# Performance work log

Hardware: AMD Instinct MI355X
Metric: run time of the kernel (lower is better)

Reference implementation:

```python
import jax, jax.numpy as jnp
import numpy as np

BLK = 128            # weight_block_size for w8a16 blockwise dequant
H = 1024             # hidden_size
I = 512              # moe_intermediate_size
E = 64               # n_routed_experts
T = 512              # tokens (seq_len)
K = 6                # num_experts_per_tok
G = 8                # n_group
TG = 3               # topk_group
NSH = 2              # n_shared_experts
I2 = I * NSH         # shared expert intermediate size
ROUTED_SCALE = 2.5
NORM_TOPK = True


def dq(w_int8, scale, blk=BLK):
    """Blockwise w8a16 dequant: w [..., M, N] int8, scale [..., M/blk, N/blk] f32."""
    *lead, M, N = w_int8.shape
    w = w_int8.astype(scale.dtype).reshape(*lead, M // blk, blk, N // blk, blk)
    return (w * scale[..., :, None, :, None]).reshape(*lead, M, N)


def setup_inputs() -> dict:
    key = jax.random.key(0)
    ks = jax.random.split(key, 16)
    ri = lambda k, shp: jax.random.randint(k, shp, -8, 8, dtype=jnp.int8)
    rs = lambda k, shp: jax.random.uniform(k, shp, minval=0.01, maxval=0.03, dtype=jnp.float32)
    return {
        "x": jax.random.normal(ks[0], (T, H), jnp.float32),
        "gate_w": jax.random.normal(ks[1], (E, H), jnp.float32) * 0.02,  # router gate [E,H]
        "wg": ri(ks[2], (E, I, H)),  "sg": rs(ks[3], (E, I // BLK, H // BLK)),
        "wu": ri(ks[4], (E, I, H)),  "su": rs(ks[5], (E, I // BLK, H // BLK)),
        "wd": ri(ks[6], (E, I, H)),  "sd": rs(ks[7], (E, I // BLK, H // BLK)),  # down, transposed layout [I,H]
        "sh_wg": ri(ks[8], (I2, H)),  "sh_sg": rs(ks[9], (I2 // BLK, H // BLK)),
        "sh_wu": ri(ks[10], (I2, H)), "sh_su": rs(ks[11], (I2 // BLK, H // BLK)),
        "sh_wd": ri(ks[12], (I2, H)), "sh_sd": rs(ks[13], (I2 // BLK, H // BLK)),
    }


def _moe(x, gate_w, wg, sg, wu, su, wd, sd, sh_wg, sh_sg, sh_wu, sh_su, sh_wd, sh_sd):
    Tn = x.shape[0]
    # --- router: sigmoid scoring + group-limited top-k ---
    scores = jax.nn.sigmoid(x @ gate_w.T)                       # [T, E]
    gsz = E // G
    group_scores = scores.reshape(Tn, G, gsz).max(axis=-1)      # [T, G]
    _, gidx = jax.lax.top_k(group_scores, TG)                   # [T, TG]
    gmask = jax.nn.one_hot(gidx, G, dtype=scores.dtype).sum(1)  # [T, G]
    emask = jnp.repeat(gmask, gsz, axis=-1)                     # [T, E]
    masked = jnp.where(emask > 0, scores, -jnp.inf)
    w, idx = jax.lax.top_k(masked, K)                           # [T, K]
    if NORM_TOPK:
        w = w / (w.sum(-1, keepdims=True) + 1e-20)
    w = w * ROUTED_SCALE
    # per-token combine weights over experts
    comb = (jax.nn.one_hot(idx, E, dtype=x.dtype) * w[:, :, None]).sum(1)  # [T, E]

    # --- routed experts: dequantized silu-gated MLPs, masked dense combine ---
    Wg, Wu, Wd = dq(wg, sg), dq(wu, su), dq(wd, sd)             # [E, I, H]
    g = jnp.einsum('th,eih->eti', x, Wg)                        # [E, T, I]
    u = jnp.einsum('th,eih->eti', x, Wu)
    hmid = jax.nn.silu(g) * u
    y = jnp.einsum('eti,eih->eth', hmid, Wd)                    # [E, T, H]
    routed = jnp.einsum('eth,te->th', y, comb)                  # [T, H]

    # --- shared experts MLP ---
    Sg, Su, Sd = dq(sh_wg, sh_sg), dq(sh_wu, sh_su), dq(sh_wd, sh_sd)
    shared = (jax.nn.silu(x @ Sg.T) * (x @ Su.T)) @ Sd          # [T, H]
    return routed + shared


def reference(x, gate_w, wg, sg, wu, su, wd, sd, sh_wg, sh_sg, sh_wu, sh_su, sh_wd, sh_sd):
    return _moe(x, gate_w, wg, sg, wu, su, wd, sd,
                sh_wg, sh_sg, sh_wu, sh_su, sh_wd, sh_sd)
```

## Files before the change

### kernel.cpp

```cpp
#include <hip/hip_runtime.h>
#include <math.h>
#include <stdint.h>

#define T_   512
#define H_   1024
#define I_   512
#define E_   64
#define K_   6
#define G_   8
#define TG_  3
#define EB_  72

typedef _Float16 h8 __attribute__((ext_vector_type(8)));
typedef _Float16 h4v __attribute__((ext_vector_type(4)));
typedef float    f4 __attribute__((ext_vector_type(4)));

__global__ __launch_bounds__(64) void router_k(
    const float* __restrict__ x, const float* __restrict__ gw,
    int* __restrict__ cnt, int* __restrict__ tlist, float* __restrict__ wlist)
{
  const int t   = blockIdx.x;
  const int tid = threadIdx.x;
  __shared__ float sx[H_];
  __shared__ float sc[E_];

  for (int h4 = tid; h4 < H_/4; h4 += 64)
    ((float4*)sx)[h4] = ((const float4*)(x + (size_t)t*H_))[h4];
  __syncthreads();

  const float* wr = gw + (size_t)tid * H_;
  float acc = 0.f;
  for (int h = 0; h < H_; h += 4) {
    float4 xv = *(const float4*)(sx + h);
    float4 wv = *(const float4*)(wr + h);
    acc = fmaf(xv.x, wv.x, acc); acc = fmaf(xv.y, wv.y, acc);
    acc = fmaf(xv.z, wv.z, acc); acc = fmaf(xv.w, wv.w, acc);
  }
  sc[tid] = 1.f / (1.f + expf(-acc));
  __syncthreads();

  if (tid == 0) {
    float gs[G_];
    #pragma unroll
    for (int g = 0; g < G_; g++) {
      float m = sc[g*8];
      #pragma unroll
      for (int j = 1; j < 8; j++) m = fmaxf(m, sc[g*8+j]);
      gs[g] = m;
    }
    unsigned gp = 0;
    for (int r = 0; r < TG_; r++) {
      int best = 0; float bv = -1e30f;
      for (int g = 0; g < G_; g++)
        if (!((gp >> g) & 1) && gs[g] > bv) { bv = gs[g]; best = g; }
      gp |= 1u << best;
    }
    int   eidx[K_]; float ew[K_];
    unsigned long long em = 0ull;
    float wsum = 0.f;
    for (int r = 0; r < K_; r++) {
      int best = 0; float bv = -1e30f;
      for (int e = 0; e < E_; e++) {
        if (!((gp >> (e >> 3)) & 1)) continue;
        if ((em >> e) & 1ull) continue;
        if (sc[e] > bv) { bv = sc[e]; best = e; }
      }
      em |= 1ull << best; eidx[r] = best; ew[r] = bv; wsum += bv;
    }
    const float inv = 2.5f / (wsum + 1e-20f);
    for (int r = 0; r < K_; r++) {
      int e = eidx[r];
      int pos = atomicAdd(&cnt[e], 1);
      tlist[e*T_ + pos] = (t << 13) | (t*K_ + r);
      wlist[e*T_ + pos] = ew[r] * inv;
    }
  }
}

__global__ void pseudo_init_k(int* cnt, int* tlist, float* wlist) {
  int s = blockIdx.x*256 + threadIdx.x;
  if (s == 0) { cnt[64] = T_; cnt[65] = T_; }
  if (s < 1024) {
    int e = 64 + (s >> 9);
    int t = s & 511;
    tlist[e*T_ + t] = (t << 13) | (3072 + s);
    wlist[e*T_ + t] = 1.0f;
  }
}

__global__ __launch_bounds__(256) void xh_prep_k(
    const float* __restrict__ x, _Float16* __restrict__ xh)
{
  int i = blockIdx.x*256 + threadIdx.x;
  float4 v = ((const float4*)x)[i];
  h4v o = { (_Float16)v.x, (_Float16)v.y, (_Float16)v.z, (_Float16)v.w };
  *(h4v*)(xh + (size_t)i*4) = o;
}

__device__ __forceinline__ void eb_decode(int eb, const int* cnt,
                                          int& e, int& lo, int& hi) {
  if (eb < E_) { e = eb; lo = 0; hi = cnt[e]; }
  else { int q = (eb - E_) & 3; e = E_ + ((eb - E_) >> 2); lo = q*128; hi = lo + 128; }
}

__device__ __forceinline__ h8 bfrag(const int* __restrict__ p, float s) {
  int4 a = *(const int4*)(p);
  int4 b = *(const int4*)(p + 4);
  union { _Float16 f[8]; h8 v; } t;
  t.f[0]=(_Float16)((float)a.x*s); t.f[1]=(_Float16)((float)a.y*s);
  t.f[2]=(_Float16)((float)a.z*s); t.f[3]=(_Float16)((float)a.w*s);
  t.f[4]=(_Float16)((float)b.x*s); t.f[5]=(_Float16)((float)b.y*s);
  t.f[6]=(_Float16)((float)b.z*s); t.f[7]=(_Float16)((float)b.w*s);
  return t.v;
}

__global__ __launch_bounds__(256) void gateup_k(
    const _Float16* __restrict__ xh,
    const int* __restrict__ wg, const float* __restrict__ sg,
    const int* __restrict__ wu, const float* __restrict__ su,
    const int* __restrict__ shwg, const float* __restrict__ shsg,
    const int* __restrict__ shwu, const float* __restrict__ shsu,
    const int* __restrict__ cnt, const int* __restrict__ tlist,
    const float* __restrict__ wlist,
    _Float16* __restrict__ hmid)
{
  const int ic = blockIdx.x;
  const int eb = blockIdx.y;
  int e, lo, hi;
  eb_decode(eb, cnt, e, lo, hi);
  if (hi <= lo) return;

  const int tid  = threadIdx.x;
  const int lane = tid & 63;
  const int wv   = tid >> 6;
  const int mr   = lane & 15;
  const int quad = lane >> 4;

  const int *wgb, *wub; const float *sgp, *sup; int sib;
  if (e < E_) {
    wgb = wg + (size_t)e*I_*H_;  wub = wu + (size_t)e*I_*H_;
    sgp = sg + e*32;  sup = su + e*32;  sib = ic >> 1;
  } else {
    int hf = e - E_;
    wgb = shwg + (size_t)hf*512*H_;  wub = shwu + (size_t)hf*512*H_;
    sgp = shsg;  sup = shsu;  sib = hf*4 + (ic >> 1);
  }
  float scg[8], scu[8];
  #pragma unroll
  for (int hb = 0; hb < 8; hb++) { scg[hb] = sgp[sib*8+hb]; scu[hb] = sup[sib*8+hb]; }

  const int r0 = ic*64 + wv*16 + mr;
  const int* gp = wgb + (size_t)r0*H_;
  const int* up = wub + (size_t)r0*H_;

  __shared__ int   stok[64];
  __shared__ int   srow[64];
  __shared__ float swt[64];

  for (int base = lo; base < hi; base += 64) {
    __syncthreads();
    if (tid < 64) {
      int slot = base + tid;
      if (slot < hi) {
        int ent = tlist[e*T_ + slot];
        stok[tid] = ent >> 13; srow[tid] = ent & 8191; swt[tid] = wlist[e*T_ + slot];
      } else { stok[tid] = -1; srow[tid] = 0; swt[tid] = 0.f; }
    }
    __syncthreads();

    const _Float16* ax[4];
    #pragma unroll
    for (int mt = 0; mt < 4; mt++) {
      int tok = stok[mt*16 + mr];
      ax[mt] = xh + (size_t)(tok < 0 ? 0 : tok) * H_ + quad*8;
    }

    f4 accg[4], accu[4];
    #pragma unroll
    for (int mt = 0; mt < 4; mt++) { accg[mt] = (f4){0.f,0.f,0.f,0.f}; accu[mt] = accg[mt]; }

    #pragma unroll 4
    for (int kt = 0; kt < 32; kt++) {
      const int k0 = kt*32 + quad*8;
      const float sg_ = scg[kt>>2], su_ = scu[kt>>2];
      h8 bg = bfrag(gp + k0, sg_);
      h8 bu = bfrag(up + k0, su_);
      #pragma unroll
      for (int mt = 0; mt < 4; mt++) {
        h8 av = *(const h8*)(ax[mt] + kt*32);
        accg[mt] = __builtin_amdgcn_mfma_f32_16x16x32_f16(av, bg, accg[mt], 0,0,0);
        accu[mt] = __builtin_amdgcn_mfma_f32_16x16x32_f16(av, bu, accu[mt], 0,0,0);
      }
    }

    const int icol = ic*64 + wv*16 + mr;
    #pragma unroll
    for (int mt = 0; mt < 4; mt++) {
      #pragma unroll
      for (int r = 0; r < 4; r++) {
        int sl = mt*16 + quad*4 + r;
        if (stok[sl] >= 0) {
          float g = accg[mt][r];
          float m = g / (1.f + expf(-g)) * accu[mt][r] * swt[sl];
          hmid[(size_t)srow[sl]*I_ + icol] = (_Float16)m;
        }
      }
    }
  }
}

__global__ __launch_bounds__(256) void down_k(
    const int* __restrict__ wd, const float* __restrict__ sd,
    const int* __restrict__ shwd, const float* __restrict__ shsd,
    const int* __restrict__ cnt, const int* __restrict__ tlist,
    const _Float16* __restrict__ hmid, float* __restrict__ out)
{
  const int hc = blockIdx.x;
  const int eb = blockIdx.y;
  int e, lo, hi;
  eb_decode(eb, cnt, e, lo, hi);
  if (hi <= lo) return;

  const int tid  = threadIdx.x;
  const int lane = tid & 63;
  const int wv   = tid >> 6;
  const int mr   = lane & 15;
  const int quad = lane >> 4;

  const int* wb; const float* sdp; int sib0;
  if (e < E_) { wb = wd + (size_t)e*I_*H_;        sdp = sd + e*32;  sib0 = 0; }
  else { int hf = e - E_; wb = shwd + (size_t)hf*512*H_; sdp = shsd; sib0 = hf*4; }
  float scd[4];
  #pragma unroll
  for (int ib = 0; ib < 4; ib++) scd[ib] = sdp[(sib0+ib)*8 + hc];

  const int hcol0 = hc*128 + wv*32 + mr;
  const int* bcol0 = wb + hcol0;

  __shared__ int stok[64];
  __shared__ int srow[64];

  for (int base = lo; base < hi; base += 64) {
    __syncthreads();
    if (tid < 64) {
      int slot = base + tid;
      if (slot < hi) {
        int ent = tlist[e*T_ + slot];
        stok[tid] = ent >> 13; srow[tid] = ent & 8191;
      } else { stok[tid] = -1; srow[tid] = 0; }
    }
    __syncthreads();

    const _Float16* ap[4];
    #pragma unroll
    for (int mt = 0; mt < 4; mt++)
      ap[mt] = hmid + (size_t)srow[mt*16 + mr]*I_ + quad*8;

    f4 a0[4], a1[4];
    #pragma unroll
    for (int mt = 0; mt < 4; mt++) { a0[mt] = (f4){0.f,0.f,0.f,0.f}; a1[mt] = a0[mt]; }

    #pragma unroll 2
    for (int kt = 0; kt < 16; kt++) {
      const float s = scd[kt>>2];
      const size_t ib0 = (size_t)(kt*32 + quad*8) * H_;
      union { _Float16 f[8]; h8 v; } b0, b1;
      #pragma unroll
      for (int j = 0; j < 8; j++) {
        b0.f[j] = (_Float16)((float)bcol0[ib0 + (size_t)j*H_     ] * s);
        b1.f[j] = (_Float16)((float)bcol0[ib0 + (size_t)j*H_ + 16] * s);
      }
      #pragma unroll
      for (int mt = 0; mt < 4; mt++) {
        h8 av = *(const h8*)(ap[mt] + kt*32);
        a0[mt] = __builtin_amdgcn_mfma_f32_16x16x32_f16(av, b0.v, a0[mt], 0,0,0);
        a1[mt] = __builtin_amdgcn_mfma_f32_16x16x32_f16(av, b1.v, a1[mt], 0,0,0);
      }
    }

    #pragma unroll
    for (int mt = 0; mt < 4; mt++) {
      #pragma unroll
      for (int p = 0; p < 2; p++) {
        f4 av2 = (p == 0) ? a0[mt] : a1[mt];
        const int hcol = hcol0 + p*16;
        #pragma unroll
        for (int r = 0; r < 4; r++) {
          int sl = mt*16 + quad*4 + r;
          int t = stok[sl];
          if (t >= 0) atomicAdd(out + (size_t)t*H_ + hcol, av2[r]);
        }
      }
    }
  }
}

extern "C" void kernel_launch(void* const* d_in, const int* in_sizes, int n_in,
                              void* d_out, int out_size, void* d_ws, size_t ws_size,
                              hipStream_t stream) {
  (void)in_sizes; (void)n_in; (void)ws_size;
  const float* x    = (const float*)d_in[0];
  const float* gw   = (const float*)d_in[1];
  const int*   wg   = (const int*  )d_in[2];
  const float* sg   = (const float*)d_in[3];
  const int*   wu   = (const int*  )d_in[4];
  const float* su   = (const float*)d_in[5];
  const int*   wd   = (const int*  )d_in[6];
  const float* sd   = (const float*)d_in[7];
  const int*   shwg = (const int*  )d_in[8];
  const float* shsg = (const float*)d_in[9];
  const int*   shwu = (const int*  )d_in[10];
  const float* shsu = (const float*)d_in[11];
  const int*   shwd = (const int*  )d_in[12];
  const float* shsd = (const float*)d_in[13];
  float* out = (float*)d_out;

  char* ws = (char*)d_ws;
  int*      cnt   = (int*     ) ws;
  int*      tlist = (int*     )(ws + 1024);
  float*    wlist = (float*   )(ws + 1024 + 66*T_*4);
  _Float16* hmid  = (_Float16*)(ws + 1024 + 2*66*T_*4);
  _Float16* xh    = (_Float16*)(ws + 1024 + 2*66*T_*4 + 4096*I_*2);

  hipMemsetAsync(cnt, 0, 1024, stream);
  hipMemsetAsync(d_out, 0, (size_t)out_size * sizeof(float), stream);
  xh_prep_k<<<T_*H_/1024, 256, 0, stream>>>(x, xh);
  router_k<<<T_, 64, 0, stream>>>(x, gw, cnt, tlist, wlist);
  pseudo_init_k<<<4, 256, 0, stream>>>(cnt, tlist, wlist);
  gateup_k<<<dim3(8, EB_), 256, 0, stream>>>(xh, wg, sg, wu, su,
                                             shwg, shsg, shwu, shsu,
                                             cnt, tlist, wlist, hmid);
  down_k<<<dim3(8, EB_), 256, 0, stream>>>(wd, sd, shwd, shsd,
                                           cnt, tlist, hmid, out);
}
```

Measured before the change: 541.1 us.

## Pipeline weight loads through LDS and replace atomics with scratch-slot combine

```diff
diff --git a/kernel.cpp b/kernel.cpp
--- a/kernel.cpp
+++ b/kernel.cpp
@@ -9,7 +9,7 @@
 #define K_   6
 #define G_   8
 #define TG_  3
-#define EB_  72
+#define EB_  80
 
 typedef _Float16 h8 __attribute__((ext_vector_type(8)));
 typedef _Float16 h4v __attribute__((ext_vector_type(4)));
@@ -100,12 +100,16 @@
 __device__ __forceinline__ void eb_decode(int eb, const int* cnt,
                                           int& e, int& lo, int& hi) {
   if (eb < E_) { e = eb; lo = 0; hi = cnt[e]; }
-  else { int q = (eb - E_) & 3; e = E_ + ((eb - E_) >> 2); lo = q*128; hi = lo + 128; }
-}
-
-__device__ __forceinline__ h8 bfrag(const int* __restrict__ p, float s) {
-  int4 a = *(const int4*)(p);
-  int4 b = *(const int4*)(p + 4);
+  else { int q = (eb - E_) & 7; e = E_ + ((eb - E_) >> 3); lo = q*64; hi = lo + 64; }
+}
+
+__device__ __forceinline__ void gld16(const int* g, void* l) {
+  __builtin_amdgcn_global_load_lds(
+      (const __attribute__((address_space(1))) void*)g,
+      (__attribute__((address_space(3))) void*)l, 16, 0, 0);
+}
+
+__device__ __forceinline__ h8 cvt8(int4 a, int4 b, float s) {
   union { _Float16 f[8]; h8 v; } t;
   t.f[0]=(_Float16)((float)a.x*s); t.f[1]=(_Float16)((float)a.y*s);
   t.f[2]=(_Float16)((float)a.z*s); t.f[3]=(_Float16)((float)a.w*s);
@@ -114,7 +118,12 @@
   return t.v;
 }
 
-__global__ __launch_bounds__(256) void gateup_k(
+#define WAITV8() do { asm volatile("s_waitcnt vmcnt(8)" ::: "memory"); \
+                      __builtin_amdgcn_sched_barrier(0); } while (0)
+#define WAITV4() do { asm volatile("s_waitcnt vmcnt(4)" ::: "memory"); \
+                      __builtin_amdgcn_sched_barrier(0); } while (0)
+
+__global__ __launch_bounds__(256, 3) void gateup_k(
     const _Float16* __restrict__ xh,
     const int* __restrict__ wg, const float* __restrict__ sg,
     const int* __restrict__ wu, const float* __restrict__ su,
@@ -145,75 +154,114 @@
     wgb = shwg + (size_t)hf*512*H_;  wub = shwu + (size_t)hf*512*H_;
     sgp = shsg;  sup = shsu;  sib = hf*4 + (ic >> 1);
   }
-  float scg[8], scu[8];
-  #pragma unroll
-  for (int hb = 0; hb < 8; hb++) { scg[hb] = sgp[sib*8+hb]; scu[hb] = sup[sib*8+hb]; }
-
-  const int r0 = ic*64 + wv*16 + mr;
-  const int* gp = wgb + (size_t)r0*H_;
-  const int* up = wub + (size_t)r0*H_;
-
-  __shared__ int   stok[64];
-  __shared__ int   srow[64];
-  __shared__ float swt[64];
+  const int r0base = ic*64;
+
+  __shared__ int lds[4*3*1024];
+  int* wbase = lds + wv*3072;
+
+  const int srl0 = wv*16 + (lane >> 3);
+  const int srl1 = srl0 + 8;
+  const int sc0  = ((lane & 7) ^ (srl0 & 7)) * 4;
+  const int sc1  = ((lane & 7) ^ (srl1 & 7)) * 4;
+  const int* g_r0 = wgb + (size_t)(r0base + srl0)*H_ + sc0;
+  const int* g_r1 = wgb + (size_t)(r0base + srl1)*H_ + sc1;
+  const int* u_r0 = wub + (size_t)(r0base + srl0)*H_ + sc0;
+  const int* u_r1 = wub + (size_t)(r0base + srl1)*H_ + sc1;
+
+  auto stage = [&](int* d, int kt) {
+    const int k4 = kt * 32;
+    gld16(g_r0 + k4, d);
+    gld16(g_r1 + k4, d + 256);
+    gld16(u_r0 + k4, d + 512);
+    gld16(u_r1 + k4, d + 768);
+  };
+
+  f4 accg[4], accu[4];
+  const int ro = mr*32;
+  const int c0 = ((quad*2    ) ^ (mr & 7)) * 4;
+  const int c1 = ((quad*2 + 1) ^ (mr & 7)) * 4;
+
+  auto compute = [&](const int* b, int kt, h8* A) {
+    const float sg_ = sgp[sib*8 + (kt >> 2)];
+    const float su_ = sup[sib*8 + (kt >> 2)];
+    int4 g0 = *(const int4*)(b + ro + c0);
+    int4 g1 = *(const int4*)(b + ro + c1);
+    int4 u0 = *(const int4*)(b + 512 + ro + c0);
+    int4 u1 = *(const int4*)(b + 512 + ro + c1);
+    h8 bg = cvt8(g0, g1, sg_);
+    h8 bu = cvt8(u0, u1, su_);
+    #pragma unroll
+    for (int mt = 0; mt < 4; mt++) {
+      accg[mt] = __builtin_amdgcn_mfma_f32_16x16x32_f16(A[mt], bg, accg[mt], 0,0,0);
+      accu[mt] = __builtin_amdgcn_mfma_f32_16x16x32_f16(A[mt], bu, accu[mt], 0,0,0);
+    }
+  };
+
+#define GU_STEP(KT, BUFC, BUFS, AUSE, ALOAD)                                \
+    WAITV8();                                                               \
+    _Pragma("unroll")                                                       \
+    for (int mt = 0; mt < 4; mt++)                                          \
+      ALOAD[mt] = *(const h8*)(ax[mt] + ((KT)+1)*32);                       \
+    stage(wbase + (BUFS)*1024, (KT)+2);                                     \
+    compute(wbase + (BUFC)*1024, (KT), AUSE);
 
   for (int base = lo; base < hi; base += 64) {
-    __syncthreads();
-    if (tid < 64) {
-      int slot = base + tid;
-      if (slot < hi) {
-        int ent = tlist[e*T_ + slot];
-        stok[tid] = ent >> 13; srow[tid] = ent & 8191; swt[tid] = wlist[e*T_ + slot];
-      } else { stok[tid] = -1; srow[tid] = 0; swt[tid] = 0.f; }
-    }
-    __syncthreads();
-
     const _Float16* ax[4];
     #pragma unroll
     for (int mt = 0; mt < 4; mt++) {
-      int tok = stok[mt*16 + mr];
-      ax[mt] = xh + (size_t)(tok < 0 ? 0 : tok) * H_ + quad*8;
-    }
-
-    f4 accg[4], accu[4];
+      int sl = base + mt*16 + mr;
+      int tok = (sl < hi) ? (tlist[e*T_ + sl] >> 13) : 0;
+      ax[mt] = xh + (size_t)tok*H_ + quad*8;
+    }
     #pragma unroll
     for (int mt = 0; mt < 4; mt++) { accg[mt] = (f4){0.f,0.f,0.f,0.f}; accu[mt] = accg[mt]; }
 
-    #pragma unroll 4
-    for (int kt = 0; kt < 32; kt++) {
-      const int k0 = kt*32 + quad*8;
-      const float sg_ = scg[kt>>2], su_ = scu[kt>>2];
-      h8 bg = bfrag(gp + k0, sg_);
-      h8 bu = bfrag(up + k0, su_);
-      #pragma unroll
-      for (int mt = 0; mt < 4; mt++) {
-        h8 av = *(const h8*)(ax[mt] + kt*32);
-        accg[mt] = __builtin_amdgcn_mfma_f32_16x16x32_f16(av, bg, accg[mt], 0,0,0);
-        accu[mt] = __builtin_amdgcn_mfma_f32_16x16x32_f16(av, bu, accu[mt], 0,0,0);
-      }
-    }
+    h8 A0[4], A1[4];
+    stage(wbase, 0);
+    #pragma unroll
+    for (int mt = 0; mt < 4; mt++) A0[mt] = *(const h8*)(ax[mt]);
+    stage(wbase + 1024, 1);
+
+    for (int k6 = 0; k6 < 5; k6++) {
+      const int kt = k6*6;
+      GU_STEP(kt+0, 0, 2, A0, A1)
+      GU_STEP(kt+1, 1, 0, A1, A0)
+      GU_STEP(kt+2, 2, 1, A0, A1)
+      GU_STEP(kt+3, 0, 2, A1, A0)
+      GU_STEP(kt+4, 1, 0, A0, A1)
+      GU_STEP(kt+5, 2, 1, A1, A0)
+    }
+    WAITV8();
+    #pragma unroll
+    for (int mt = 0; mt < 4; mt++) A1[mt] = *(const h8*)(ax[mt] + 31*32);
+    compute(wbase, 30, A0);
+    WAITV4();
+    compute(wbase + 1024, 31, A1);
 
     const int icol = ic*64 + wv*16 + mr;
     #pragma unroll
     for (int mt = 0; mt < 4; mt++) {
       #pragma unroll
       for (int r = 0; r < 4; r++) {
-        int sl = mt*16 + quad*4 + r;
-        if (stok[sl] >= 0) {
+        int sl = base + mt*16 + quad*4 + r;
+        if (sl < hi) {
+          int   ent = tlist[e*T_ + sl];
+          float wt  = wlist[e*T_ + sl];
           float g = accg[mt][r];
-          float m = g / (1.f + expf(-g)) * accu[mt][r] * swt[sl];
-          hmid[(size_t)srow[sl]*I_ + icol] = (_Float16)m;
+          float m = g / (1.f + expf(-g)) * accu[mt][r] * wt;
+          hmid[(size_t)(ent & 8191)*I_ + icol] = (_Float16)m;
         }
       }
     }
   }
-}
-
-__global__ __launch_bounds__(256) void down_k(
+#undef GU_STEP
+}
+
+__global__ __launch_bounds__(256, 2) void down_k(
     const int* __restrict__ wd, const float* __restrict__ sd,
     const int* __restrict__ shwd, const float* __restrict__ shsd,
     const int* __restrict__ cnt, const int* __restrict__ tlist,
-    const _Float16* __restrict__ hmid, float* __restrict__ out)
+    const _Float16* __restrict__ hmid, float* __restrict__ scr)
 {
   const int hc = blockIdx.x;
   const int eb = blockIdx.y;
@@ -230,75 +278,144 @@
   const int* wb; const float* sdp; int sib0;
   if (e < E_) { wb = wd + (size_t)e*I_*H_;        sdp = sd + e*32;  sib0 = 0; }
   else { int hf = e - E_; wb = shwd + (size_t)hf*512*H_; sdp = shsd; sib0 = hf*4; }
-  float scd[4];
-  #pragma unroll
-  for (int ib = 0; ib < 4; ib++) scd[ib] = sdp[(sib0+ib)*8 + hc];
-
-  const int hcol0 = hc*128 + wv*32 + mr;
-  const int* bcol0 = wb + hcol0;
-
-  __shared__ int stok[64];
-  __shared__ int srow[64];
+
+  __shared__ _Float16 dlds[4][2][2048];
+  _Float16* l0 = &dlds[wv][0][0];
+  _Float16* l1 = &dlds[wv][1][0];
+
+  const int h0  = hc*128 + wv*32;
+  const int ig0 = lane >> 3, ig1 = ig0 + 8;
+  const int hg4 = (lane & 7) * 4;
+  const int* src0 = wb + (size_t)(ig0*4)*H_ + h0 + hg4;
+  const int* src1 = wb + (size_t)(ig1*4)*H_ + h0 + hg4;
+
+  auto dload = [&](int4* w, int kt) {
+    const size_t o = (size_t)kt * 64 * H_;
+    #pragma unroll
+    for (int j = 0; j < 4; j++) {
+      w[j]     = *(const int4*)(src0 + o + (size_t)j*H_);
+      w[4 + j] = *(const int4*)(src1 + o + (size_t)j*H_);
+    }
+  };
+
+  auto dwrite = [&](_Float16* lb, const int4* w, float s) {
+    #pragma unroll
+    for (int r = 0; r < 2; r++) {
+      const int ig = r ? ig1 : ig0;
+      #pragma unroll
+      for (int j2 = 0; j2 < 4; j2++) {
+        const int hrow = hg4 + j2;
+        const int swz  = (hrow & 7) ^ ((hrow >> 3) & 3);
+        h4v v = { (_Float16)((float)((&w[r*4+0].x)[j2]) * s),
+                  (_Float16)((float)((&w[r*4+1].x)[j2]) * s),
+                  (_Float16)((float)((&w[r*4+2].x)[j2]) * s),
+                  (_Float16)((float)((&w[r*4+3].x)[j2]) * s) };
+        *(h4v*)((char*)lb + hrow*128 + ((((ig >> 1) ^ swz)) << 4) + ((ig & 1) << 3)) = v;
+      }
+    }
+  };
+
+  f4 acc[2][4];
+  auto dcompute = [&](const _Float16* lb, h8 (&A)[4][2]) {
+    #pragma unroll
+    for (int nf = 0; nf < 2; nf++) {
+      const int hrow = nf*16 + mr;
+      const int swz  = (hrow & 7) ^ ((hrow >> 3) & 3);
+      #pragma unroll
+      for (int ks = 0; ks < 2; ks++) {
+        h8 bf = *(const h8*)((const char*)lb + hrow*128 + ((((ks << 2) + quad) ^ swz) << 4));
+        #pragma unroll
+        for (int mt = 0; mt < 4; mt++)
+          acc[nf][mt] = __builtin_amdgcn_mfma_f32_16x16x32_f16(A[mt][ks], bf, acc[nf][mt], 0,0,0);
+      }
+    }
+  };
+
+#define D_STEP(KT, AU, AL, WL, WW, LBC, LBW)                                \
+    if ((KT) < 7) {                                                         \
+      _Pragma("unroll")                                                     \
+      for (int mt = 0; mt < 4; mt++) {                                      \
+        AL[mt][0] = *(const h8*)(ap[mt] + ((KT)+1)*64);                     \
+        AL[mt][1] = *(const h8*)(ap[mt] + ((KT)+1)*64 + 32);                \
+      }                                                                     \
+    }                                                                       \
+    if ((KT) < 6) dload(WL, (KT)+2);                                        \
+    if ((KT) < 7) dwrite(LBW, WW, sdp[(sib0 + (((KT)+1) >> 1))*8 + hc]);    \
+    dcompute(LBC, AU);
 
   for (int base = lo; base < hi; base += 64) {
-    __syncthreads();
-    if (tid < 64) {
-      int slot = base + tid;
-      if (slot < hi) {
-        int ent = tlist[e*T_ + slot];
-        stok[tid] = ent >> 13; srow[tid] = ent & 8191;
-      } else { stok[tid] = -1; srow[tid] = 0; }
-    }
-    __syncthreads();
-
     const _Float16* ap[4];
     #pragma unroll
-    for (int mt = 0; mt < 4; mt++)
-      ap[mt] = hmid + (size_t)srow[mt*16 + mr]*I_ + quad*8;
-
-    f4 a0[4], a1[4];
-    #pragma unroll
-    for (int mt = 0; mt < 4; mt++) { a0[mt] = (f4){0.f,0.f,0.f,0.f}; a1[mt] = a0[mt]; }
-
-    #pragma unroll 2
-    for (int kt = 0; kt < 16; kt++) {
-      const float s = scd[kt>>2];
-      const size_t ib0 = (size_t)(kt*32 + quad*8) * H_;
-      union { _Float16 f[8]; h8 v; } b0, b1;
-      #pragma unroll
-      for (int j = 0; j < 8; j++) {
-        b0.f[j] = (_Float16)((float)bcol0[ib0 + (size_t)j*H_     ] * s);
-        b1.f[j] = (_Float16)((float)bcol0[ib0 + (size_t)j*H_ + 16] * s);
-      }
-      #pragma unroll
-      for (int mt = 0; mt < 4; mt++) {
-        h8 av = *(const h8*)(ap[mt] + kt*32);
-        a0[mt] = __builtin_amdgcn_mfma_f32_16x16x32_f16(av, b0.v, a0[mt], 0,0,0);
-        a1[mt] = __builtin_amdgcn_mfma_f32_16x16x32_f16(av, b1.v, a1[mt], 0,0,0);
-      }
-    }
-
-    #pragma unroll
-    for (int mt = 0; mt < 4; mt++) {
-      #pragma unroll
-      for (int p = 0; p < 2; p++) {
-        f4 av2 = (p == 0) ? a0[mt] : a1[mt];
-        const int hcol = hcol0 + p*16;
-        #pragma unroll
-        for (int r = 0; r < 4; r++) {
-          int sl = mt*16 + quad*4 + r;
-          int t = stok[sl];
-          if (t >= 0) atomicAdd(out + (size_t)t*H_ + hcol, av2[r]);
+    for (int mt = 0; mt < 4; mt++) {
+      int sl = base + mt*16 + mr;
+      int sr = (sl < hi) ? (tlist[e*T_ + sl] & 8191) : 0;
+      ap[mt] = hmid + (size_t)sr*I_ + quad*8;
+    }
+    #pragma unroll
+    for (int nf = 0; nf < 2; nf++)
+      #pragma unroll
+      for (int mt = 0; mt < 4; mt++) acc[nf][mt] = (f4){0.f,0.f,0.f,0.f};
+
+    h8 avvA[4][2], avvB[4][2];
+    int4 wA[8], wB[8];
+    #pragma unroll
+    for (int mt = 0; mt < 4; mt++) {
+      avvA[mt][0] = *(const h8*)(ap[mt]);
+      avvA[mt][1] = *(const h8*)(ap[mt] + 32);
+    }
+    dload(wA, 0);
+    dload(wB, 1);
+    dwrite(l0, wA, sdp[sib0*8 + hc]);
+
+    D_STEP(0, avvA, avvB, wA, wB, l0, l1)
+    D_STEP(1, avvB, avvA, wB, wA, l1, l0)
+    D_STEP(2, avvA, avvB, wA, wB, l0, l1)
+    D_STEP(3, avvB, avvA, wB, wA, l1, l0)
+    D_STEP(4, avvA, avvB, wA, wB, l0, l1)
+    D_STEP(5, avvB, avvA, wB, wA, l1, l0)
+    D_STEP(6, avvA, avvB, wA, wB, l0, l1)
+    D_STEP(7, avvB, avvA, wB, wA, l1, l0)
+
+    #pragma unroll
+    for (int mt = 0; mt < 4; mt++) {
+      #pragma unroll
+      for (int r = 0; r < 4; r++) {
+        int sl = base + mt*16 + quad*4 + r;
+        if (sl < hi) {
+          int ent = tlist[e*T_ + sl];
+          int t   = ent >> 13;
+          int sr  = ent & 8191;
+          int rank = (sr < 3072) ? (sr - t*6) : (6 + ((sr - 3072) >> 9));
+          float* dst = scr + (size_t)(t*8 + rank)*H_ + h0 + mr;
+          dst[0]  = acc[0][mt][r];
+          dst[16] = acc[1][mt][r];
         }
       }
     }
   }
+#undef D_STEP
+}
+
+__global__ __launch_bounds__(256) void combine_k(
+    const float* __restrict__ scr, float* __restrict__ out)
+{
+  int i = blockIdx.x*256 + threadIdx.x;
+  int t = i >> 8;
+  int c = i & 255;
+  const float4* base = (const float4*)(scr + (size_t)t*8*H_) + c;
+  float4 s = base[0];
+  #pragma unroll
+  for (int r = 1; r < 8; r++) {
+    float4 v = base[(size_t)r*(H_/4)];
+    s.x += v.x; s.y += v.y; s.z += v.z; s.w += v.w;
+  }
+  ((float4*)out)[i] = s;
 }
 
 extern "C" void kernel_launch(void* const* d_in, const int* in_sizes, int n_in,
                               void* d_out, int out_size, void* d_ws, size_t ws_size,
                               hipStream_t stream) {
-  (void)in_sizes; (void)n_in; (void)ws_size;
+  (void)in_sizes; (void)n_in; (void)ws_size; (void)out_size;
   const float* x    = (const float*)d_in[0];
   const float* gw   = (const float*)d_in[1];
   const int*   wg   = (const int*  )d_in[2];
@@ -321,9 +438,9 @@
   float*    wlist = (float*   )(ws + 1024 + 66*T_*4);
   _Float16* hmid  = (_Float16*)(ws + 1024 + 2*66*T_*4);
   _Float16* xh    = (_Float16*)(ws + 1024 + 2*66*T_*4 + 4096*I_*2);
+  float*    scr   = (float*   )(ws + 1024 + 2*66*T_*4 + 4096*I_*2 + T_*H_*2);
 
   hipMemsetAsync(cnt, 0, 1024, stream);
-  hipMemsetAsync(d_out, 0, (size_t)out_size * sizeof(float), stream);
   xh_prep_k<<<T_*H_/1024, 256, 0, stream>>>(x, xh);
   router_k<<<T_, 64, 0, stream>>>(x, gw, cnt, tlist, wlist);
   pseudo_init_k<<<4, 256, 0, stream>>>(cnt, tlist, wlist);
@@ -331,5 +448,6 @@
                                              shwg, shsg, shwu, shsu,
                                              cnt, tlist, wlist, hmid);
   down_k<<<dim3(8, EB_), 256, 0, stream>>>(wd, sd, shwd, shsd,
-                                           cnt, tlist, hmid, out);
-}
+                                           cnt, tlist, hmid, scr);
+  combine_k<<<T_*H_/1024, 256, 0, stream>>>(scr, out);
+}
```

New measurement: 520.6 us. 3.8% less time.
